# Optimization experiments

Hardware: AMD Instinct MI355X
Metric: run time of the kernel (lower is better)

## Reference

```python
import jax, jax.numpy as jnp
import numpy as np
from jax import lax

N, M, K, D = 2048, 64, 32, 512
C = 1.0


def setup_inputs() -> dict:
    key = jax.random.key(0)
    k1, k2, k3, k4 = jax.random.split(key, 4)
    W = jax.random.normal(k1, (K, D), dtype=jnp.float32) * 0.05
    T = jax.random.normal(k2, (K, K), dtype=jnp.float32) * 0.05
    data = jax.random.normal(k3, (N, M, D), dtype=jnp.float32)
    labels = jax.random.randint(k4, (N, M), 0, K, dtype=jnp.int32)
    return {"W": W, "T": T, "data": data, "labels": labels}


def _crf_word(W, T, data, labels):
    # data: [m, d], labels: [m] int. dots: [m, K] emission scores.
    dots = data @ W.T
    m = dots.shape[0]
    k = T.shape[0]

    # alpha[i, k] = logsumexp_j(dots[i-1, j] + alpha[i-1, j] + T[j, k]); alpha[0] = 0
    def alpha_step(prev, d_prev):
        a = jax.nn.logsumexp(prev[:, None] + d_prev[:, None] + T, axis=0)
        return a, a
    _, alphas = lax.scan(alpha_step, jnp.zeros((k,), dots.dtype), dots[:-1])
    alpha = jnp.concatenate([jnp.zeros((1, k), dots.dtype), alphas], axis=0)  # [m, K]

    # beta[i, k] = logsumexp_j(dots[i+1, j] + beta[i+1, j] + T[k, j]); beta[m-1] = 0
    def beta_step(prev, d_next):
        b = jax.nn.logsumexp(prev[None, :] + d_next[None, :] + T, axis=1)
        return b, b
    _, betas = lax.scan(beta_step, jnp.zeros((k,), dots.dtype), dots[1:][::-1])
    beta = jnp.concatenate([betas[::-1], jnp.zeros((1, k), dots.dtype)], axis=0)  # [m, K]

    # unary marginals p1 [m, K]
    p1 = jax.nn.softmax(alpha + beta + dots, axis=-1)
    # pairwise marginals p2 [m-1, K, K]; softmax over flattened KxK per position
    s = (alpha[:-1] + dots[:-1])[:, :, None] + (beta[1:] + dots[1:])[:, None, :] + T[None, :, :]
    p2 = jax.nn.softmax(s.reshape(m - 1, k * k), axis=-1).reshape(m - 1, k, k)

    # log P(y|x)
    logZ = jax.nn.logsumexp(dots[-1] + alpha[-1])
    emit = jnp.take_along_axis(dots, labels[:, None], axis=1).sum()
    trans = T[labels[:-1], labels[1:]].sum()
    logpyx = emit + trans - logZ

    # analytic gradients (as computed by the module, not autodiff)
    onehot = jax.nn.one_hot(labels, k, dtype=dots.dtype)          # [m, K]
    dw = (onehot - p1).T @ data                                    # [K, d]
    trans_oh = onehot[:-1][:, :, None] * onehot[1:][:, None, :]    # [m-1, K, K]
    dT = (trans_oh - p2).sum(axis=0)                               # [K, K]
    return logpyx, dw, dT


def reference(W, T, data, labels):
    logpyx, dw, dT = jax.vmap(_crf_word, in_axes=(None, None, 0, 0))(W, T, data, labels)
    meandw = dw.mean(axis=0)
    meandT = dT.mean(axis=0)
    gradients = jnp.concatenate([meandw.ravel(), meandT.ravel()])
    # objValue (stored on the module) -- computed for faithfulness though forward returns gradients
    obj = -C * logpyx.mean() + 0.5 * jnp.sum(W ** 2) + 0.5 * jnp.sum(T ** 2)
    del obj
    return gradients
```

## Files before the change

kernel.cpp:

```cpp
#include <hip/hip_runtime.h>
#include <math.h>

typedef __bf16 bf16x8 __attribute__((ext_vector_type(8)));
typedef float f32x4 __attribute__((ext_vector_type(4)));

__device__ __forceinline__ bf16x8 to_bf16x8(float4 a, float4 b) {
    bf16x8 r;
    r[0] = (__bf16)a.x; r[1] = (__bf16)a.y; r[2] = (__bf16)a.z; r[3] = (__bf16)a.w;
    r[4] = (__bf16)b.x; r[5] = (__bf16)b.y; r[6] = (__bf16)b.z; r[7] = (__bf16)b.w;
    return r;
}
#define MFMA16(A, B, C) __builtin_amdgcn_mfma_f32_16x16x32_bf16((A), (B), (C), 0, 0, 0)

__device__ __forceinline__ float rsum32(float v) {
    v += __shfl_xor(v, 1, 32); v += __shfl_xor(v, 2, 32);
    v += __shfl_xor(v, 4, 32); v += __shfl_xor(v, 8, 32);
    v += __shfl_xor(v, 16, 32);
    return v;
}

__device__ __forceinline__ float rl(float v, int j) {
    return __int_as_float(__builtin_amdgcn_readlane(__float_as_int(v), j));
}
#define RL_MATVEC(T, EV, OUT)                                                  \
    {                                                                          \
        float a0_ = 0.f, a1_ = 0.f, a2_ = 0.f, a3_ = 0.f;                      \
        _Pragma("unroll") for (int j_ = 0; j_ < 32; j_ += 4) {                 \
            a0_ += EV[j_ + 0] * rl((T), j_ + 0);                               \
            a1_ += EV[j_ + 1] * rl((T), j_ + 1);                               \
            a2_ += EV[j_ + 2] * rl((T), j_ + 2);                               \
            a3_ += EV[j_ + 3] * rl((T), j_ + 3);                               \
        }                                                                      \
        OUT = (a0_ + a1_) + (a2_ + a3_);                                       \
    }

__global__ __launch_bounds__(256) void k_prep(const float* __restrict__ W,
                                              bf16x8* __restrict__ wsW) {
    const int e = blockIdx.x * 256 + threadIdx.x;
    const int gk = e >> 7, h = (e >> 6) & 1, l = e & 63;
    const float* src = W + (size_t)(h * 16 + (l & 15)) * 512 + gk * 32 + (l >> 4) * 8;
    float4 lo = *(const float4*)src, hi = *(const float4*)(src + 4);
    wsW[e] = to_bf16x8(lo, hi);
}

__global__ __launch_bounds__(256) void k_dots_gd(const float* __restrict__ data,
                                                 const bf16x8* __restrict__ wsW,
                                                 __bf16* __restrict__ gdg) {
    const int tid = threadIdx.x;
    const int w = tid >> 6;
    const int lane = tid & 63;
    const int m16 = lane & 15;
    const int kb = lane >> 4;
    const size_t row0 = (size_t)blockIdx.x * 128 + w * 32;
    const float* arow0 = data + (row0 + m16) * 512 + kb * 8;
    const float* arow1 = arow0 + 16 * 512;

    f32x4 acc00 = {0.f, 0.f, 0.f, 0.f}, acc01 = {0.f, 0.f, 0.f, 0.f};
    f32x4 acc10 = {0.f, 0.f, 0.f, 0.f}, acc11 = {0.f, 0.f, 0.f, 0.f};

#pragma unroll 2
    for (int kk = 0; kk < 16; ++kk) {
        const int off = kk * 32;
        float4 a0l = *(const float4*)(arow0 + off);
        float4 a0h = *(const float4*)(arow0 + off + 4);
        float4 a1l = *(const float4*)(arow1 + off);
        float4 a1h = *(const float4*)(arow1 + off + 4);
        bf16x8 a0 = to_bf16x8(a0l, a0h), a1 = to_bf16x8(a1l, a1h);
        bf16x8 b0 = wsW[kk * 128 + lane];
        bf16x8 b1 = wsW[kk * 128 + 64 + lane];
        acc00 = MFMA16(a0, b0, acc00);
        acc01 = MFMA16(a0, b1, acc01);
        acc10 = MFMA16(a1, b0, acc10);
        acc11 = MFMA16(a1, b1, acc11);
    }
    __bf16* ob = gdg + (row0 + kb * 4) * 32 + m16;
#pragma unroll
    for (int r = 0; r < 4; ++r) {
        ob[r * 32]            = (__bf16)__expf(acc00[r]);
        ob[r * 32 + 16]       = (__bf16)__expf(acc01[r]);
        ob[512 + r * 32]      = (__bf16)__expf(acc10[r]);
        ob[512 + r * 32 + 16] = (__bf16)__expf(acc11[r]);
    }
}

__global__ __launch_bounds__(128) void k_fb(const __bf16* __restrict__ gdg,
                                            const float* __restrict__ Tm,
                                            const int* __restrict__ labels,
                                            float* __restrict__ Pdiff,
                                            float* __restrict__ dTpart) {
    __shared__ __align__(16) __bf16 gdb[2048];
    __shared__ __align__(16) __bf16 Unb[2048];
    __shared__ __align__(16) __bf16 Mb[2048];
    __shared__ float Sb[1024];
    __shared__ float bscale[64];
    __shared__ int lab[64];

    const int n = blockIdx.x;
    const int tid = threadIdx.x;
    const int wv = tid >> 6;
    const int lane = tid & 63;
    const int k = tid & 31;
    const int hw = tid >> 5;
    float* drow = Pdiff + (size_t)n * 2048;

    {
        const bf16x8* src = (const bf16x8*)(gdg + (size_t)n * 2048);
        bf16x8* dst = (bf16x8*)gdb;
        dst[tid] = src[tid];
        dst[tid + 128] = src[tid + 128];
    }
#pragma unroll
    for (int i = 0; i < 8; ++i) Sb[tid * 8 + i] = 0.f;
    if (tid < 64) { lab[tid] = labels[n * 64 + tid]; bscale[tid] = 1.f; }
    __syncthreads();

    if (wv == 0) {
        float Ecol[32];
#pragma unroll
        for (int j = 0; j < 32; ++j) Ecol[j] = __expf(Tm[j * 32 + k]);
        float Areg = 1.f;
        float gdc = (float)gdb[k];
#pragma unroll 1
        for (int g = 0; g < 16; ++g) {
#pragma unroll
            for (int ii = 0; ii < 4; ++ii) {
                const int i = g * 4 + ii;
                float t = Areg * gdc;
                Unb[i * 32 + k] = (__bf16)t;
                if (i < 63) {
                    gdc = (float)gdb[(i + 1) * 32 + k];
                    float anew;
                    RL_MATVEC(t, Ecol, anew);
                    Areg = anew;
                }
            }
            if (g < 15) Areg *= __builtin_amdgcn_rcpf(rsum32(Areg));
        }
    } else {
        float Erow[32];
#pragma unroll
        for (int j = 0; j < 32; ++j) Erow[j] = __expf(Tm[k * 32 + j]);
        float Mreg = 1.f;
        Mb[63 * 32 + k] = (__bf16)1.f;
        float gdc = (float)gdb[63 * 32 + k];
#pragma unroll 1
        for (int g = 0; g < 16; ++g) {
#pragma unroll
            for (int ii = 0; ii < 4; ++ii) {
                const int s = g * 4 + ii;
                if (s < 63) {
                    const int i = 63 - s;
                    float ww = gdc * Mreg;
                    gdc = (float)gdb[(i - 1) * 32 + k];
                    float m2;
                    RL_MATVEC(ww, Erow, m2);
                    Mb[(i - 1) * 32 + k] = (__bf16)m2;
                    Mreg = m2;
                }
            }
            if (g < 15) {
                float rc = __builtin_amdgcn_rcpf(rsum32(Mreg));
                Mreg *= rc;
                if (lane == 0) bscale[58 - 4 * g] = rc;
            }
        }
    }
    __syncthreads();

    float Scol[32];
#pragma unroll
    for (int j = 0; j < 32; ++j) Scol[j] = 0.f;
    const int i0 = hw * 16;
    for (int ii = 0; ii < 16; ++ii) {
        const int i = i0 + ii;
        float un = (float)Unb[i * 32 + k];
        float mm = (float)Mb[i * 32 + k];
        float t = un * mm;
        float Z = rsum32(t);
        float rZ = __builtin_amdgcn_rcpf(Z);
        float pd = ((lab[i] == k) ? 1.f : 0.f) - t * rZ;
        drow[i * 32 + k] = pd;
        if (i < 63) {
            float f = (float)gdb[(i + 1) * 32 + k] * (float)Mb[(i + 1) * 32 + k]
                      * rZ * bscale[i];
            const bf16x8* uv = (const bf16x8*)(&Unb[i * 32]);
            bf16x8 u0 = uv[0], u1 = uv[1], u2 = uv[2], u3 = uv[3];
#pragma unroll
            for (int j = 0; j < 8; ++j) Scol[j]      += (float)u0[j] * f;
#pragma unroll
            for (int j = 0; j < 8; ++j) Scol[8 + j]  += (float)u1[j] * f;
#pragma unroll
            for (int j = 0; j < 8; ++j) Scol[16 + j] += (float)u2[j] * f;
#pragma unroll
            for (int j = 0; j < 8; ++j) Scol[24 + j] += (float)u3[j] * f;
        }
    }
#pragma unroll
    for (int j = 0; j < 32; ++j) atomicAdd(&Sb[j * 32 + k], Scol[j]);
    __syncthreads();

    float* op = dTpart + (size_t)n * 1024;
#pragma unroll
    for (int e = 0; e < 8; ++e) {
        const int idx = tid * 8 + e;
        op[idx] = -__expf(Tm[idx]) * Sb[idx];
    }
    __syncthreads();
    if (tid < 63) atomicAdd(&op[lab[tid] * 32 + lab[tid + 1]], 1.0f);
}

__global__ __launch_bounds__(256) void k_dw(const float* __restrict__ data,
                                            const float* __restrict__ Pd,
                                            float* __restrict__ dwp) {
    const int g = blockIdx.x >> 2;
    const int q = blockIdx.x & 3;
    const int tid = threadIdx.x;
    const int kg = __builtin_amdgcn_readfirstlane(tid >> 6);
    const int lane = tid & 63;
    const int k0 = kg << 3;
    const int d0 = q * 128 + lane * 2;

    float2 acc[8];
#pragma unroll
    for (int i = 0; i < 8; ++i) acc[i] = make_float2(0.f, 0.f);

    const size_t rbase = (size_t)g * 512;
    const float* dptr = data + rbase * 512 + d0;
    const float4* pptr = (const float4*)(Pd + rbase * 32) + kg * 2;

#define FMA8_2(PA, PB, DV)                                                     \
    acc[0].x += (PA).x * (DV).x; acc[0].y += (PA).x * (DV).y;                  \
    acc[1].x += (PA).y * (DV).x; acc[1].y += (PA).y * (DV).y;                  \
    acc[2].x += (PA).z * (DV).x; acc[2].y += (PA).z * (DV).y;                  \
    acc[3].x += (PA).w * (DV).x; acc[3].y += (PA).w * (DV).y;                  \
    acc[4].x += (PB).x * (DV).x; acc[4].y += (PB).x * (DV).y;                  \
    acc[5].x += (PB).y * (DV).x; acc[5].y += (PB).y * (DV).y;                  \
    acc[6].x += (PB).z * (DV).x; acc[6].y += (PB).z * (DV).y;                  \
    acc[7].x += (PB).w * (DV).x; acc[7].y += (PB).w * (DV).y;

    for (int r = 0; r < 512; r += 4) {
        float2 dv0 = *(const float2*)(dptr + (size_t)(r + 0) * 512);
        float2 dv1 = *(const float2*)(dptr + (size_t)(r + 1) * 512);
        float2 dv2 = *(const float2*)(dptr + (size_t)(r + 2) * 512);
        float2 dv3 = *(const float2*)(dptr + (size_t)(r + 3) * 512);
        float4 pa0 = pptr[(r + 0) * 8], pb0 = pptr[(r + 0) * 8 + 1];
        float4 pa1 = pptr[(r + 1) * 8], pb1 = pptr[(r + 1) * 8 + 1];
        float4 pa2 = pptr[(r + 2) * 8], pb2 = pptr[(r + 2) * 8 + 1];
        float4 pa3 = pptr[(r + 3) * 8], pb3 = pptr[(r + 3) * 8 + 1];
        FMA8_2(pa0, pb0, dv0)
        FMA8_2(pa1, pb1, dv1)
        FMA8_2(pa2, pb2, dv2)
        FMA8_2(pa3, pb3, dv3)
    }
#undef FMA8_2

    float* op = dwp + (size_t)g * 16384;
#pragma unroll
    for (int kk = 0; kk < 8; ++kk)
        *(float2*)(op + (k0 + kk) * 512 + d0) = acc[kk];
}

__global__ __launch_bounds__(256) void k_final(const float* __restrict__ dwp,
                                               const float* __restrict__ dTp,
                                               float* __restrict__ out) {
    __shared__ float red[256];
    const int b = blockIdx.x, t = threadIdx.x;
    const float inv = 1.0f / 2048.0f;
    if (b < 256) {
        const int q = t >> 6, ol = t & 63;
        const int oi = b * 64 + ol;
        float s = 0.f;
#pragma unroll 4
        for (int j = 0; j < 64; ++j) s += dwp[(size_t)(q * 64 + j) * 16384 + oi];
        red[t] = s;
        __syncthreads();
        if (t < 64) out[b * 64 + t] = (red[t] + red[t + 64] + red[t + 128] + red[t + 192]) * inv;
    } else {
        const int ol = t >> 4, q = t & 15;
        const int oi = (b - 256) * 16 + ol;
        float s = 0.f;
#pragma unroll 4
        for (int j = 0; j < 128; ++j) s += dTp[(size_t)(q * 128 + j) * 1024 + oi];
        s += __shfl_xor(s, 1, 16); s += __shfl_xor(s, 2, 16);
        s += __shfl_xor(s, 4, 16); s += __shfl_xor(s, 8, 16);
        if (q == 0) out[16384 + oi] = s * inv;
    }
}

extern "C" void kernel_launch(void* const* d_in, const int* in_sizes, int n_in,
                              void* d_out, int out_size, void* d_ws, size_t ws_size,
                              hipStream_t stream) {
    const float* W = (const float*)d_in[0];
    const float* Tm = (const float*)d_in[1];
    const float* data = (const float*)d_in[2];
    const int* labels = (const int*)d_in[3];
    float* out = (float*)d_out;
    float* ws = (float*)d_ws;

    float* Pdiff = ws;
    float* dTpart = ws + 4194304;
    float* dwpart = ws + 6291456;
    __bf16* gdg = (__bf16*)(ws + 6291456);
    bf16x8* wsW = (bf16x8*)(ws + 10485760);

    hipLaunchKernelGGL(k_prep, dim3(8), dim3(256), 0, stream, W, wsW);
    hipLaunchKernelGGL(k_dots_gd, dim3(1024), dim3(256), 0, stream, data, wsW, gdg);
    hipLaunchKernelGGL(k_fb, dim3(2048), dim3(128), 0, stream, gdg, Tm, labels, Pdiff, dTpart);
    hipLaunchKernelGGL(k_dw, dim3(1024), dim3(256), 0, stream, data, Pdiff, dwpart);
    hipLaunchKernelGGL(k_final, dim3(320), dim3(256), 0, stream, dwpart, dTpart, out);
}
```

Measured before the change: 248.8 us.

## Double-buffer data tiles via global_load_lds with swizzled LDS layout in dots GEMM

The emission GEMM kernel now stages each 32x32 fp32 tile of data into LDS with direct global-to-LDS async loads, double-buffered per wave, and prefetches the next k-slice while computing the current one. The LDS layout is XOR-swizzled to avoid bank conflicts, and the W prep layout changes so k-index pairs match the new split of each MFMA operand into two float4s. This targets global-load latency in a memory-bound streaming GEMM, at the cost of LDS traffic, hand-written waitcnt and the risk of layout mismatch.

New measurement: 252.4 us. About the same (+1.5%).

```diff
diff --git a/kernel.cpp b/kernel.cpp
--- a/kernel.cpp
+++ b/kernel.cpp
@@ -3,6 +3,13 @@
 
 typedef __bf16 bf16x8 __attribute__((ext_vector_type(8)));
 typedef float f32x4 __attribute__((ext_vector_type(4)));
+
+typedef const __attribute__((address_space(1))) void* gas_ptr;
+typedef __attribute__((address_space(3))) void* las_ptr;
+
+__device__ __forceinline__ void gl_lds16(const float* g, float* l) {
+    __builtin_amdgcn_global_load_lds((gas_ptr)g, (las_ptr)l, 16, 0, 0);
+}
 
 __device__ __forceinline__ bf16x8 to_bf16x8(float4 a, float4 b) {
     bf16x8 r;
@@ -38,41 +45,73 @@
                                               bf16x8* __restrict__ wsW) {
     const int e = blockIdx.x * 256 + threadIdx.x;
     const int gk = e >> 7, h = (e >> 6) & 1, l = e & 63;
-    const float* src = W + (size_t)(h * 16 + (l & 15)) * 512 + gk * 32 + (l >> 4) * 8;
-    float4 lo = *(const float4*)src, hi = *(const float4*)(src + 4);
+    const int kb = l >> 4;
+    const float* src = W + (size_t)(h * 16 + (l & 15)) * 512 + gk * 32 + kb * 4;
+    float4 lo = *(const float4*)src;
+    float4 hi = *(const float4*)(src + 16);
     wsW[e] = to_bf16x8(lo, hi);
 }
 
 __global__ __launch_bounds__(256) void k_dots_gd(const float* __restrict__ data,
                                                  const bf16x8* __restrict__ wsW,
                                                  __bf16* __restrict__ gdg) {
+    __shared__ __align__(16) float stage[4][2][32][32];
     const int tid = threadIdx.x;
     const int w = tid >> 6;
     const int lane = tid & 63;
     const int m16 = lane & 15;
     const int kb = lane >> 4;
+    const int rsub = lane >> 3;
+    const int seg = lane & 7;
+    const int sw = m16 & 7;
     const size_t row0 = (size_t)blockIdx.x * 128 + w * 32;
-    const float* arow0 = data + (row0 + m16) * 512 + kb * 8;
-    const float* arow1 = arow0 + 16 * 512;
 
     f32x4 acc00 = {0.f, 0.f, 0.f, 0.f}, acc01 = {0.f, 0.f, 0.f, 0.f};
     f32x4 acc10 = {0.f, 0.f, 0.f, 0.f}, acc11 = {0.f, 0.f, 0.f, 0.f};
 
-#pragma unroll 2
+#define STAGE(BUF, KK)                                                         \
+    {                                                                          \
+        _Pragma("unroll") for (int i_ = 0; i_ < 4; ++i_) {                     \
+            gl_lds16(data + (row0 + i_ * 8 + rsub) * 512 + (KK) * 32 +         \
+                         ((seg ^ rsub) << 2),                                  \
+                     &stage[w][BUF][i_ * 8][0]);                               \
+        }                                                                      \
+    }
+
+#define COMPUTE(BUF, KK)                                                       \
+    {                                                                          \
+        const float* sb_ = &stage[w][BUF][0][0];                               \
+        float4 x0_ = *(const float4*)(sb_ + m16 * 32 + ((kb ^ sw) << 2));      \
+        float4 x1_ = *(const float4*)(sb_ + m16 * 32 + (((kb + 4) ^ sw) << 2));\
+        float4 y0_ = *(const float4*)(sb_ + (16 + m16) * 32 + ((kb ^ sw) << 2));\
+        float4 y1_ = *(const float4*)(sb_ + (16 + m16) * 32 +                  \
+                                      (((kb + 4) ^ sw) << 2));                 \
+        bf16x8 a0_ = to_bf16x8(x0_, x1_);                                      \
+        bf16x8 a1_ = to_bf16x8(y0_, y1_);                                      \
+        bf16x8 b0_ = wsW[(KK) * 128 + lane];                                   \
+        bf16x8 b1_ = wsW[(KK) * 128 + 64 + lane];                              \
+        acc00 = MFMA16(a0_, b0_, acc00);                                       \
+        acc01 = MFMA16(a0_, b1_, acc01);                                       \
+        acc10 = MFMA16(a1_, b0_, acc10);                                       \
+        acc11 = MFMA16(a1_, b1_, acc11);                                       \
+    }
+
+    STAGE(0, 0);
+#pragma unroll 1
     for (int kk = 0; kk < 16; ++kk) {
-        const int off = kk * 32;
-        float4 a0l = *(const float4*)(arow0 + off);
-        float4 a0h = *(const float4*)(arow0 + off + 4);
-        float4 a1l = *(const float4*)(arow1 + off);
-        float4 a1h = *(const float4*)(arow1 + off + 4);
-        bf16x8 a0 = to_bf16x8(a0l, a0h), a1 = to_bf16x8(a1l, a1h);
-        bf16x8 b0 = wsW[kk * 128 + lane];
-        bf16x8 b1 = wsW[kk * 128 + 64 + lane];
-        acc00 = MFMA16(a0, b0, acc00);
-        acc01 = MFMA16(a0, b1, acc01);
-        acc10 = MFMA16(a1, b0, acc10);
-        acc11 = MFMA16(a1, b1, acc11);
-    }
+        const int cur = kk & 1;
+        if (kk < 15) {
+            STAGE(cur ^ 1, kk + 1);
+            asm volatile("s_waitcnt vmcnt(4)" ::: "memory");
+        } else {
+            asm volatile("s_waitcnt vmcnt(0)" ::: "memory");
+        }
+        __builtin_amdgcn_sched_barrier(0);
+        COMPUTE(cur, kk);
+    }
+#undef STAGE
+#undef COMPUTE
+
     __bf16* ob = gdg + (row0 + kb * 4) * 32 + m16;
 #pragma unroll
     for (int r = 0; r < 4; ++r) {
```
